# Optimization experiments

Measured on AMD Instinct MI355X. Metric: run time of the kernel, lower is better.

## Reference

```python
import jax, jax.numpy as jnp
import numpy as np
from jax import lax

ANCHOR_NUM = 5
OUTPUT_NUM = 4  # 'reg' branch


def setup_inputs() -> dict:
    key = jax.random.key(0)
    k1, k2 = jax.random.split(key)
    detection = jax.random.normal(k1, (64, 20, 20, 256), dtype=jnp.float32)
    templates = jax.random.normal(k2, (64, 4, 4, 256 * ANCHOR_NUM * OUTPUT_NUM), dtype=jnp.float32)
    return {"detection": detection, "templates": templates}


def reference(detection, templates):
    # detection: [B, Hd, Wd, C]; templates: [B, Hk, Wk, C * O]
    # Original TF code fakes per-example-kernel conv via one big depthwise_conv2d
    # followed by reduce_sum over channel groups. Mathematically:
    #   out[b, y, x, o] = sum_{i,j,c} detection[b, y+i, x+j, c] * tmpl[b, i, j, c, o]
    # i.e. a per-example VALID cross-correlation. We express it as a vmapped conv.
    B, Hd, Wd, C = detection.shape
    _, Hk, Wk, CO = templates.shape
    O = CO // C  # anchor_num * output_num = 20
    tmpl = templates.reshape(B, Hk, Wk, C, O)

    def corr_one(det, ker):
        # det: [Hd, Wd, C], ker: [Hk, Wk, C, O] -> [Ho, Wo, O]
        out = lax.conv_general_dilated(
            det[None],  # [1, Hd, Wd, C]
            ker,        # HWIO
            window_strides=(1, 1),
            padding="VALID",
            dimension_numbers=("NHWC", "HWIO", "NHWC"),
        )
        return out[0]

    out = jax.vmap(corr_one)(detection, tmpl)  # [B, Ho, Wo, O]
    return out
```

## Files before the change

kernel.cpp:

```cpp
#include <hip/hip_runtime.h>
#include <hip/hip_bf16.h>


typedef __bf16 bf16x8 __attribute__((ext_vector_type(8)));
typedef float f32x4 __attribute__((ext_vector_type(4)));

#define NB 64
#define C_TOT 256
#define CQ 32
#define NQ 8
#define NPOS 400
#define NP 289
#define NPP 296
#define NO 20
#define OPAD 20
#define QSTRIDE (NB * NO * NPP)
#define DET_LDS_BYTES (NPOS * CQ * 2)
#define TMP_LDS_BYTES (16 * OPAD * CQ * 2)

__device__ __forceinline__ unsigned short bfbits(float f) {
  __bf16 h = (__bf16)f;
  return __builtin_bit_cast(unsigned short, h);
}
__device__ __forceinline__ unsigned pk2(float a, float b) {
  return (unsigned)bfbits(a) | ((unsigned)bfbits(b) << 16);
}
__device__ __forceinline__ float lo2f(unsigned u) {
  return __builtin_bit_cast(float, u << 16);
}
__device__ __forceinline__ float hi2f(unsigned u) {
  return __builtin_bit_cast(float, u & 0xFFFF0000u);
}

__global__ __launch_bounds__(256)
void reduce_kernel(const unsigned short* __restrict__ ws, float* __restrict__ out) {
  __shared__ float sbuf[NO * 80];
  const int b    = blockIdx.x >> 2;
  const int pg   = blockIdx.x & 3;
  const int p0g  = pg * 80;
  const int np   = (NP - p0g < 80) ? (NP - p0g) : 80;
  const int noct = (np + 7) >> 3;
  const int units = NO * noct;

  const int t = threadIdx.x;
  if (t < units) {
    int o  = t / noct;
    int po = t - o * noct;
    const unsigned short* src = ws + ((size_t)b * NO + o) * NPP + p0g + po * 8;
    float s[8] = {0, 0, 0, 0, 0, 0, 0, 0};
    #pragma unroll
    for (int q = 0; q < NQ; ++q) {
      uint4 v = *(const uint4*)(src + (size_t)q * QSTRIDE);
      s[0] += lo2f(v.x); s[1] += hi2f(v.x);
      s[2] += lo2f(v.y); s[3] += hi2f(v.y);
      s[4] += lo2f(v.z); s[5] += hi2f(v.z);
      s[6] += lo2f(v.w); s[7] += hi2f(v.w);
    }
    #pragma unroll
    for (int j = 0; j < 8; ++j) sbuf[o * 80 + po * 8 + j] = s[j];
  }
  __syncthreads();

  for (int p = t; p < np; p += 256) {
    float* dst = out + (size_t)b * (NP * NO) + (p0g + p) * NO;
    #pragma unroll
    for (int k = 0; k < 5; ++k) {
      f32x4 v;
      #pragma unroll
      for (int j = 0; j < 4; ++j) v[j] = sbuf[(k * 4 + j) * 80 + p];
      *(f32x4*)(dst + k * 4) = v;
    }
  }
}

__global__ __launch_bounds__(512, 2)
void siamese_kernel(const float* __restrict__ det,
                    const float* __restrict__ tmp,
                    unsigned short* __restrict__ ws) {
  __shared__ alignas(16) char lds[DET_LDS_BYTES + TMP_LDS_BYTES];
  char* detB = lds;
  char* tmpB = lds + DET_LDS_BYTES;

  const int tid = threadIdx.x;
  const int b   = blockIdx.x >> 3;
  const int q   = blockIdx.x & 7;
  const int c0  = q * CQ;

  const float* __restrict__ dsrc = det + (size_t)b * (NPOS * C_TOT) + c0;
  const float* __restrict__ tsrc = tmp + (size_t)b * (16 * C_TOT * NO);

  float4 dva[4][2];
  int dpos[4] = {0, 0, 0, 0}, dcp[4] = {0, 0, 0, 0};
  #pragma unroll
  for (int k = 0; k < 3; ++k) {
    int u = tid + k * 512;
    dpos[k] = u >> 2; dcp[k] = u & 3;
    const float* s = dsrc + dpos[k] * C_TOT + dcp[k] * 8;
    dva[k][0] = *(const float4*)s;
    dva[k][1] = *(const float4*)(s + 4);
  }
  if (tid < 64) {
    int u = 1536 + tid;
    dpos[3] = u >> 2; dcp[3] = u & 3;
    const float* s = dsrc + dpos[3] * C_TOT + dcp[3] * 8;
    dva[3][0] = *(const float4*)s;
    dva[3][1] = *(const float4*)(s + 4);
  }
  int t_ij = 0, t_co = 0, t_oq = 0;
  float4 tv[8];
  if (tid < 320) {
    t_ij = tid / 20;
    int r = tid - t_ij * 20;
    t_co = r / 5;
    t_oq = r - t_co * 5;
    const float* s = tsrc + t_ij * (C_TOT * NO) + (c0 + t_co * 8) * NO + t_oq * 4;
    #pragma unroll
    for (int rr = 0; rr < 8; ++rr) tv[rr] = *(const float4*)(s + rr * NO);
  }

  #pragma unroll
  for (int k = 0; k < 3; ++k) {
    uint4 w = { pk2(dva[k][0].x, dva[k][0].y), pk2(dva[k][0].z, dva[k][0].w),
                pk2(dva[k][1].x, dva[k][1].y), pk2(dva[k][1].z, dva[k][1].w) };
    *(uint4*)(detB + dpos[k] * 64 + ((dcp[k] ^ ((dpos[k] >> 1) & 3)) << 4)) = w;
  }
  if (tid < 64) {
    uint4 w = { pk2(dva[3][0].x, dva[3][0].y), pk2(dva[3][0].z, dva[3][0].w),
                pk2(dva[3][1].x, dva[3][1].y), pk2(dva[3][1].z, dva[3][1].w) };
    *(uint4*)(detB + dpos[3] * 64 + ((dcp[3] ^ ((dpos[3] >> 1) & 3)) << 4)) = w;
  }
  if (tid < 320) {
    char* base = tmpB + t_ij * (OPAD * 64);
    #pragma unroll
    for (int k = 0; k < 4; ++k) {
      int o = t_oq * 4 + k;
      uint4 w;
      #define COMP(V) ((k == 0) ? (V).x : (k == 1) ? (V).y : (k == 2) ? (V).z : (V).w)
      w.x = pk2(COMP(tv[0]), COMP(tv[1]));
      w.y = pk2(COMP(tv[2]), COMP(tv[3]));
      w.z = pk2(COMP(tv[4]), COMP(tv[5]));
      w.w = pk2(COMP(tv[6]), COMP(tv[7]));
      #undef COMP
      *(uint4*)(base + o * 64 + ((t_co ^ ((o >> 1) & 3)) << 4)) = w;
    }
  }

  __syncthreads();

  const int w    = tid >> 6;
  const int lane = tid & 63;
  const int lo   = lane & 15;
  const int hi   = lane >> 4;
  const int nm   = (w < 3) ? 3 : 2;

  int posb[3];
  #pragma unroll
  for (int mi = 0; mi < 3; ++mi) {
    int m = w + mi * 8;
    int p = m * 16 + lo;
    if (p > NP - 1) p = NP - 1;
    posb[mi] = (p / 17) * 20 + (p % 17);
  }

  f32x4 acc[3][2] = {};

  const int o0r  = lo;
  const int o1r  = (16 + lo < NO) ? (16 + lo) : (NO - 1);
  const int bad0 = o0r * 64 + ((hi ^ ((o0r >> 1) & 3)) << 4);
  const int bad1 = o1r * 64 + ((hi ^ ((o1r >> 1) & 3)) << 4);

  for (int ij = 0; ij < 16; ++ij) {
    const int sh = (ij >> 2) * 20 + (ij & 3);

    bf16x8 bf0 = *(const bf16x8*)(tmpB + bad0 + ij * (OPAD * 64));
    bf16x8 bf1 = *(const bf16x8*)(tmpB + bad1 + ij * (OPAD * 64));

    #pragma unroll
    for (int mi = 0; mi < 3; ++mi) {
      if (mi < nm) {
        int pos  = posb[mi] + sh;
        int byte = pos * 64 + ((hi ^ ((pos >> 1) & 3)) << 4);
        bf16x8 a = *(const bf16x8*)(detB + byte);
        acc[mi][0] = __builtin_amdgcn_mfma_f32_16x16x32_bf16(a, bf0, acc[mi][0], 0, 0, 0);
        acc[mi][1] = __builtin_amdgcn_mfma_f32_16x16x32_bf16(a, bf1, acc[mi][1], 0, 0, 0);
      }
    }
  }

  unsigned short* __restrict__ pws = ws + ((size_t)q * NB + b) * (NO * NPP);
  #pragma unroll
  for (int mi = 0; mi < 3; ++mi) {
    if (mi < nm) {
      int p0 = (w + mi * 8) * 16 + hi * 4;
      #pragma unroll
      for (int n = 0; n < 2; ++n) {
        int o = n * 16 + lo;
        if (o < NO) {
          if (p0 + 4 <= NP) {
            uint2 val = { pk2(acc[mi][n][0], acc[mi][n][1]),
                          pk2(acc[mi][n][2], acc[mi][n][3]) };
            *(uint2*)(pws + o * NPP + p0) = val;
          } else if (p0 < NP) {
            pws[o * NPP + p0] = bfbits(acc[mi][n][0]);
          }
        }
      }
    }
  }
}

extern "C" void kernel_launch(void* const* d_in, const int* in_sizes, int n_in,
                              void* d_out, int out_size, void* d_ws, size_t ws_size,
                              hipStream_t stream) {
  (void)in_sizes; (void)n_in; (void)out_size; (void)ws_size;
  const float* det = (const float*)d_in[0];
  const float* tmp = (const float*)d_in[1];
  float* out = (float*)d_out;
  unsigned short* ws = (unsigned short*)d_ws;

  siamese_kernel<<<dim3(NB * NQ), dim3(512), 0, stream>>>(det, tmp, ws);
  reduce_kernel<<<dim3(NB * 4), dim3(256), 0, stream>>>(ws, out);
}
```

Measured before the change: 21.92 us.

## Split output rows into two halves per block to double grid size

Each block now handles one channel quarter for half of the output rows (tiles 0-9 or 10-18) and loads only the needed detection rows (13 or 11 rows with halo) into LDS. The grid grows from 512 to 1024 blocks, and launch bounds now ask for 8 blocks per CU. The goal is more parallelism and occupancy across the 256 CUs and less LDS per block. The cost is that the template slice and the overlapping halo rows are loaded twice, and each block has less work to hide latency.

```diff
diff --git a/kernel.cpp b/kernel.cpp
--- a/kernel.cpp
+++ b/kernel.cpp
@@ -9,13 +9,12 @@
 #define C_TOT 256
 #define CQ 32
 #define NQ 8
-#define NPOS 400
 #define NP 289
 #define NPP 296
 #define NO 20
 #define OPAD 20
 #define QSTRIDE (NB * NO * NPP)
-#define DET_LDS_BYTES (NPOS * CQ * 2)
+#define DET_LDS_BYTES (13 * 20 * CQ * 2)
 #define TMP_LDS_BYTES (16 * OPAD * CQ * 2)
 
 __device__ __forceinline__ unsigned short bfbits(float f) {
@@ -73,7 +72,7 @@
   }
 }
 
-__global__ __launch_bounds__(512, 2)
+__global__ __launch_bounds__(512, 8)
 void siamese_kernel(const float* __restrict__ det,
                     const float* __restrict__ tmp,
                     unsigned short* __restrict__ ws) {
@@ -82,54 +81,36 @@
   char* tmpB = lds + DET_LDS_BYTES;
 
   const int tid = threadIdx.x;
-  const int b   = blockIdx.x >> 3;
-  const int q   = blockIdx.x & 7;
+  const int idx = blockIdx.x;
+  const int b   = idx >> 4;
+  const int q   = idx & 7;
+  const int h   = (idx >> 3) & 1;
   const int c0  = q * CQ;
-
-  const float* __restrict__ dsrc = det + (size_t)b * (NPOS * C_TOT) + c0;
+  const int y0  = h * 9;
+  const int nry = h ? 11 : 13;
+
+  const float* __restrict__ dsrc = det + (size_t)b * (400 * C_TOT)
+                                   + (y0 * 20) * C_TOT + c0;
   const float* __restrict__ tsrc = tmp + (size_t)b * (16 * C_TOT * NO);
 
-  float4 dva[4][2];
-  int dpos[4] = {0, 0, 0, 0}, dcp[4] = {0, 0, 0, 0};
-  #pragma unroll
-  for (int k = 0; k < 3; ++k) {
-    int u = tid + k * 512;
-    dpos[k] = u >> 2; dcp[k] = u & 3;
-    const float* s = dsrc + dpos[k] * C_TOT + dcp[k] * 8;
-    dva[k][0] = *(const float4*)s;
-    dva[k][1] = *(const float4*)(s + 4);
-  }
-  if (tid < 64) {
-    int u = 1536 + tid;
-    dpos[3] = u >> 2; dcp[3] = u & 3;
-    const float* s = dsrc + dpos[3] * C_TOT + dcp[3] * 8;
-    dva[3][0] = *(const float4*)s;
-    dva[3][1] = *(const float4*)(s + 4);
-  }
-  int t_ij = 0, t_co = 0, t_oq = 0;
-  float4 tv[8];
+  for (int u = tid; u < nry * 20 * 4; u += 512) {
+    int lp = u >> 2, cp = u & 3;
+    const float* s = dsrc + lp * C_TOT + cp * 8;
+    float4 A = *(const float4*)s;
+    float4 B = *(const float4*)(s + 4);
+    uint4 w = { pk2(A.x, A.y), pk2(A.z, A.w), pk2(B.x, B.y), pk2(B.z, B.w) };
+    *(uint4*)(detB + lp * 64 + ((cp ^ ((lp >> 1) & 3)) << 4)) = w;
+  }
+
   if (tid < 320) {
-    t_ij = tid / 20;
-    int r = tid - t_ij * 20;
-    t_co = r / 5;
-    t_oq = r - t_co * 5;
+    int t_ij = tid / 20;
+    int r    = tid - t_ij * 20;
+    int t_co = r / 5;
+    int t_oq = r - t_co * 5;
     const float* s = tsrc + t_ij * (C_TOT * NO) + (c0 + t_co * 8) * NO + t_oq * 4;
+    float4 tv[8];
     #pragma unroll
     for (int rr = 0; rr < 8; ++rr) tv[rr] = *(const float4*)(s + rr * NO);
-  }
-
-  #pragma unroll
-  for (int k = 0; k < 3; ++k) {
-    uint4 w = { pk2(dva[k][0].x, dva[k][0].y), pk2(dva[k][0].z, dva[k][0].w),
-                pk2(dva[k][1].x, dva[k][1].y), pk2(dva[k][1].z, dva[k][1].w) };
-    *(uint4*)(detB + dpos[k] * 64 + ((dcp[k] ^ ((dpos[k] >> 1) & 3)) << 4)) = w;
-  }
-  if (tid < 64) {
-    uint4 w = { pk2(dva[3][0].x, dva[3][0].y), pk2(dva[3][0].z, dva[3][0].w),
-                pk2(dva[3][1].x, dva[3][1].y), pk2(dva[3][1].z, dva[3][1].w) };
-    *(uint4*)(detB + dpos[3] * 64 + ((dcp[3] ^ ((dpos[3] >> 1) & 3)) << 4)) = w;
-  }
-  if (tid < 320) {
     char* base = tmpB + t_ij * (OPAD * 64);
     #pragma unroll
     for (int k = 0; k < 4; ++k) {
@@ -151,18 +132,19 @@
   const int lane = tid & 63;
   const int lo   = lane & 15;
   const int hi   = lane >> 4;
-  const int nm   = (w < 3) ? 3 : 2;
-
-  int posb[3];
+  const int base = h * 10;
+  const int nm   = h ? ((w == 0) ? 2 : 1) : ((w < 2) ? 2 : 1);
+
+  int posb[2];
   #pragma unroll
-  for (int mi = 0; mi < 3; ++mi) {
-    int m = w + mi * 8;
+  for (int mi = 0; mi < 2; ++mi) {
+    int m = base + w + mi * 8;
     int p = m * 16 + lo;
     if (p > NP - 1) p = NP - 1;
-    posb[mi] = (p / 17) * 20 + (p % 17);
-  }
-
-  f32x4 acc[3][2] = {};
+    posb[mi] = (p / 17 - y0) * 20 + (p % 17);
+  }
+
+  f32x4 acc[2][2] = {};
 
   const int o0r  = lo;
   const int o1r  = (16 + lo < NO) ? (16 + lo) : (NO - 1);
@@ -176,10 +158,10 @@
     bf16x8 bf1 = *(const bf16x8*)(tmpB + bad1 + ij * (OPAD * 64));
 
     #pragma unroll
-    for (int mi = 0; mi < 3; ++mi) {
+    for (int mi = 0; mi < 2; ++mi) {
       if (mi < nm) {
-        int pos  = posb[mi] + sh;
-        int byte = pos * 64 + ((hi ^ ((pos >> 1) & 3)) << 4);
+        int lpos = posb[mi] + sh;
+        int byte = lpos * 64 + ((hi ^ ((lpos >> 1) & 3)) << 4);
         bf16x8 a = *(const bf16x8*)(detB + byte);
         acc[mi][0] = __builtin_amdgcn_mfma_f32_16x16x32_bf16(a, bf0, acc[mi][0], 0, 0, 0);
         acc[mi][1] = __builtin_amdgcn_mfma_f32_16x16x32_bf16(a, bf1, acc[mi][1], 0, 0, 0);
@@ -189,9 +171,9 @@
 
   unsigned short* __restrict__ pws = ws + ((size_t)q * NB + b) * (NO * NPP);
   #pragma unroll
-  for (int mi = 0; mi < 3; ++mi) {
+  for (int mi = 0; mi < 2; ++mi) {
     if (mi < nm) {
-      int p0 = (w + mi * 8) * 16 + hi * 4;
+      int p0 = (base + w + mi * 8) * 16 + hi * 4;
       #pragma unroll
       for (int n = 0; n < 2; ++n) {
         int o = n * 16 + lo;
@@ -218,6 +200,6 @@
   float* out = (float*)d_out;
   unsigned short* ws = (unsigned short*)d_ws;
 
-  siamese_kernel<<<dim3(NB * NQ), dim3(512), 0, stream>>>(det, tmp, ws);
+  siamese_kernel<<<dim3(NB * NQ * 2), dim3(512), 0, stream>>>(det, tmp, ws);
   reduce_kernel<<<dim3(NB * 4), dim3(256), 0, stream>>>(ws, out);
 }
```

New measurement: 22.42 us. 2.3% more time.

## Process two batches per block with double-buffered LDS to overlap loads and MFMA

Applied to the files above, without the earlier changes.

Each block now handles two batch elements (b and b+32) for the same channel quarter. The global loads for the second batch are issued before computing the first, then written to a second LDS buffer, so memory latency overlaps compute. This halves the grid to 256 blocks, which is about one block per CU on a 256-CU device. It also doubles LDS per block and raises register pressure, which may reduce occupancy and parallelism.

```diff
diff --git a/kernel.cpp b/kernel.cpp
--- a/kernel.cpp
+++ b/kernel.cpp
@@ -17,6 +17,7 @@
 #define QSTRIDE (NB * NO * NPP)
 #define DET_LDS_BYTES (NPOS * CQ * 2)
 #define TMP_LDS_BYTES (16 * OPAD * CQ * 2)
+#define BUF_BYTES (DET_LDS_BYTES + TMP_LDS_BYTES)
 
 __device__ __forceinline__ unsigned short bfbits(float f) {
   __bf16 h = (__bf16)f;
@@ -73,101 +74,83 @@
   }
 }
 
-__global__ __launch_bounds__(512, 2)
-void siamese_kernel(const float* __restrict__ det,
-                    const float* __restrict__ tmp,
-                    unsigned short* __restrict__ ws) {
-  __shared__ alignas(16) char lds[DET_LDS_BYTES + TMP_LDS_BYTES];
-  char* detB = lds;
-  char* tmpB = lds + DET_LDS_BYTES;
-
-  const int tid = threadIdx.x;
-  const int b   = blockIdx.x >> 3;
-  const int q   = blockIdx.x & 7;
-  const int c0  = q * CQ;
-
-  const float* __restrict__ dsrc = det + (size_t)b * (NPOS * C_TOT) + c0;
-  const float* __restrict__ tsrc = tmp + (size_t)b * (16 * C_TOT * NO);
-
+struct StageRegs {
   float4 dva[4][2];
-  int dpos[4] = {0, 0, 0, 0}, dcp[4] = {0, 0, 0, 0};
+  float4 tv[8];
+};
+
+__device__ __forceinline__ void stage_load(const float* __restrict__ dsrc,
+                                           const float* __restrict__ tsrc,
+                                           int tid, int c0, StageRegs& r) {
   #pragma unroll
   for (int k = 0; k < 3; ++k) {
     int u = tid + k * 512;
-    dpos[k] = u >> 2; dcp[k] = u & 3;
-    const float* s = dsrc + dpos[k] * C_TOT + dcp[k] * 8;
-    dva[k][0] = *(const float4*)s;
-    dva[k][1] = *(const float4*)(s + 4);
+    const float* s = dsrc + (u >> 2) * C_TOT + (u & 3) * 8;
+    r.dva[k][0] = *(const float4*)s;
+    r.dva[k][1] = *(const float4*)(s + 4);
   }
   if (tid < 64) {
     int u = 1536 + tid;
-    dpos[3] = u >> 2; dcp[3] = u & 3;
-    const float* s = dsrc + dpos[3] * C_TOT + dcp[3] * 8;
-    dva[3][0] = *(const float4*)s;
-    dva[3][1] = *(const float4*)(s + 4);
-  }
-  int t_ij = 0, t_co = 0, t_oq = 0;
-  float4 tv[8];
+    const float* s = dsrc + (u >> 2) * C_TOT + (u & 3) * 8;
+    r.dva[3][0] = *(const float4*)s;
+    r.dva[3][1] = *(const float4*)(s + 4);
+  }
   if (tid < 320) {
-    t_ij = tid / 20;
-    int r = tid - t_ij * 20;
-    t_co = r / 5;
-    t_oq = r - t_co * 5;
+    int t_ij = tid / 20;
+    int rr_  = tid - t_ij * 20;
+    int t_co = rr_ / 5;
+    int t_oq = rr_ - t_co * 5;
     const float* s = tsrc + t_ij * (C_TOT * NO) + (c0 + t_co * 8) * NO + t_oq * 4;
     #pragma unroll
-    for (int rr = 0; rr < 8; ++rr) tv[rr] = *(const float4*)(s + rr * NO);
-  }
-
+    for (int rr = 0; rr < 8; ++rr) r.tv[rr] = *(const float4*)(s + rr * NO);
+  }
+}
+
+__device__ __forceinline__ void stage_write(char* __restrict__ detB,
+                                            char* __restrict__ tmpB,
+                                            int tid, const StageRegs& r) {
   #pragma unroll
   for (int k = 0; k < 3; ++k) {
-    uint4 w = { pk2(dva[k][0].x, dva[k][0].y), pk2(dva[k][0].z, dva[k][0].w),
-                pk2(dva[k][1].x, dva[k][1].y), pk2(dva[k][1].z, dva[k][1].w) };
-    *(uint4*)(detB + dpos[k] * 64 + ((dcp[k] ^ ((dpos[k] >> 1) & 3)) << 4)) = w;
+    int u = tid + k * 512;
+    int pos = u >> 2, cp = u & 3;
+    uint4 w = { pk2(r.dva[k][0].x, r.dva[k][0].y), pk2(r.dva[k][0].z, r.dva[k][0].w),
+                pk2(r.dva[k][1].x, r.dva[k][1].y), pk2(r.dva[k][1].z, r.dva[k][1].w) };
+    *(uint4*)(detB + pos * 64 + ((cp ^ ((pos >> 1) & 3)) << 4)) = w;
   }
   if (tid < 64) {
-    uint4 w = { pk2(dva[3][0].x, dva[3][0].y), pk2(dva[3][0].z, dva[3][0].w),
-                pk2(dva[3][1].x, dva[3][1].y), pk2(dva[3][1].z, dva[3][1].w) };
-    *(uint4*)(detB + dpos[3] * 64 + ((dcp[3] ^ ((dpos[3] >> 1) & 3)) << 4)) = w;
+    int u = 1536 + tid;
+    int pos = u >> 2, cp = u & 3;
+    uint4 w = { pk2(r.dva[3][0].x, r.dva[3][0].y), pk2(r.dva[3][0].z, r.dva[3][0].w),
+                pk2(r.dva[3][1].x, r.dva[3][1].y), pk2(r.dva[3][1].z, r.dva[3][1].w) };
+    *(uint4*)(detB + pos * 64 + ((cp ^ ((pos >> 1) & 3)) << 4)) = w;
   }
   if (tid < 320) {
+    int t_ij = tid / 20;
+    int rr_  = tid - t_ij * 20;
+    int t_co = rr_ / 5;
+    int t_oq = rr_ - t_co * 5;
     char* base = tmpB + t_ij * (OPAD * 64);
     #pragma unroll
     for (int k = 0; k < 4; ++k) {
       int o = t_oq * 4 + k;
       uint4 w;
       #define COMP(V) ((k == 0) ? (V).x : (k == 1) ? (V).y : (k == 2) ? (V).z : (V).w)
-      w.x = pk2(COMP(tv[0]), COMP(tv[1]));
-      w.y = pk2(COMP(tv[2]), COMP(tv[3]));
-      w.z = pk2(COMP(tv[4]), COMP(tv[5]));
-      w.w = pk2(COMP(tv[6]), COMP(tv[7]));
+      w.x = pk2(COMP(r.tv[0]), COMP(r.tv[1]));
+      w.y = pk2(COMP(r.tv[2]), COMP(r.tv[3]));
+      w.z = pk2(COMP(r.tv[4]), COMP(r.tv[5]));
+      w.w = pk2(COMP(r.tv[6]), COMP(r.tv[7]));
       #undef COMP
       *(uint4*)(base + o * 64 + ((t_co ^ ((o >> 1) & 3)) << 4)) = w;
     }
   }
-
-  __syncthreads();
-
-  const int w    = tid >> 6;
-  const int lane = tid & 63;
-  const int lo   = lane & 15;
-  const int hi   = lane >> 4;
-  const int nm   = (w < 3) ? 3 : 2;
-
-  int posb[3];
-  #pragma unroll
-  for (int mi = 0; mi < 3; ++mi) {
-    int m = w + mi * 8;
-    int p = m * 16 + lo;
-    if (p > NP - 1) p = NP - 1;
-    posb[mi] = (p / 17) * 20 + (p % 17);
-  }
-
+}
+
+__device__ __forceinline__ void compute_unit(const char* __restrict__ detB,
+                                             const char* __restrict__ tmpB,
+                                             int w, int lo, int hi, int nm,
+                                             const int posb[3], int bad0, int bad1,
+                                             unsigned short* __restrict__ pws) {
   f32x4 acc[3][2] = {};
-
-  const int o0r  = lo;
-  const int o1r  = (16 + lo < NO) ? (16 + lo) : (NO - 1);
-  const int bad0 = o0r * 64 + ((hi ^ ((o0r >> 1) & 3)) << 4);
-  const int bad1 = o1r * 64 + ((hi ^ ((o1r >> 1) & 3)) << 4);
 
   for (int ij = 0; ij < 16; ++ij) {
     const int sh = (ij >> 2) * 20 + (ij & 3);
@@ -187,7 +170,6 @@
     }
   }
 
-  unsigned short* __restrict__ pws = ws + ((size_t)q * NB + b) * (NO * NPP);
   #pragma unroll
   for (int mi = 0; mi < 3; ++mi) {
     if (mi < nm) {
@@ -209,6 +191,64 @@
   }
 }
 
+__global__ __launch_bounds__(512, 2)
+void siamese_kernel(const float* __restrict__ det,
+                    const float* __restrict__ tmp,
+                    unsigned short* __restrict__ ws) {
+  __shared__ alignas(16) char lds[2 * BUF_BYTES];
+
+  const int tid = threadIdx.x;
+  const int u0  = blockIdx.x;
+  const int b0  = u0 >> 3;
+  const int q   = u0 & 7;
+  const int b1  = b0 + 32;
+  const int c0  = q * CQ;
+
+  const float* dsrc0 = det + (size_t)b0 * (NPOS * C_TOT) + c0;
+  const float* tsrc0 = tmp + (size_t)b0 * (16 * C_TOT * NO);
+  const float* dsrc1 = det + (size_t)b1 * (NPOS * C_TOT) + c0;
+  const float* tsrc1 = tmp + (size_t)b1 * (16 * C_TOT * NO);
+
+  {
+    StageRegs r0;
+    stage_load(dsrc0, tsrc0, tid, c0, r0);
+    stage_write(lds, lds + DET_LDS_BYTES, tid, r0);
+  }
+  __syncthreads();
+
+  StageRegs r1;
+  stage_load(dsrc1, tsrc1, tid, c0, r1);
+
+  const int w    = tid >> 6;
+  const int lane = tid & 63;
+  const int lo   = lane & 15;
+  const int hi   = lane >> 4;
+  const int nm   = (w < 3) ? 3 : 2;
+
+  int posb[3];
+  #pragma unroll
+  for (int mi = 0; mi < 3; ++mi) {
+    int m = w + mi * 8;
+    int p = m * 16 + lo;
+    if (p > NP - 1) p = NP - 1;
+    posb[mi] = (p / 17) * 20 + (p % 17);
+  }
+  const int o0r  = lo;
+  const int o1r  = (16 + lo < NO) ? (16 + lo) : (NO - 1);
+  const int bad0 = o0r * 64 + ((hi ^ ((o0r >> 1) & 3)) << 4);
+  const int bad1 = o1r * 64 + ((hi ^ ((o1r >> 1) & 3)) << 4);
+
+  compute_unit(lds, lds + DET_LDS_BYTES, w, lo, hi, nm, posb, bad0, bad1,
+               ws + ((size_t)q * NB + b0) * (NO * NPP));
+
+  stage_write(lds + BUF_BYTES, lds + BUF_BYTES + DET_LDS_BYTES, tid, r1);
+  __syncthreads();
+
+  compute_unit(lds + BUF_BYTES, lds + BUF_BYTES + DET_LDS_BYTES, w, lo, hi, nm,
+               posb, bad0, bad1,
+               ws + ((size_t)q * NB + b1) * (NO * NPP));
+}
+
 extern "C" void kernel_launch(void* const* d_in, const int* in_sizes, int n_in,
                               void* d_out, int out_size, void* d_ws, size_t ws_size,
                               hipStream_t stream) {
@@ -218,6 +258,6 @@
   float* out = (float*)d_out;
   unsigned short* ws = (unsigned short*)d_ws;
 
-  siamese_kernel<<<dim3(NB * NQ), dim3(512), 0, stream>>>(det, tmp, ws);
+  siamese_kernel<<<dim3(NB * NQ / 2), dim3(512), 0, stream>>>(det, tmp, ws);
   reduce_kernel<<<dim3(NB * 4), dim3(256), 0, stream>>>(ws, out);
 }
```

New measurement: 23.61 us. 1.08x slower.
